# Performance work log

Hardware: AMD Instinct MI355X
Metric: run time of the kernel (lower is better)

## Reference

```python
import jax, jax.numpy as jnp
import numpy as np
from jax import lax

D, H_HEADS, DEPTH, E, HID, P, NCLS = 768, 12, 12, 4, 3072, 16, 1000

def _ln(x, w, b, eps=1e-5):
    m = x.mean(-1, keepdims=True)
    v = ((x - m) ** 2).mean(-1, keepdims=True)
    return (x - m) * lax.rsqrt(v + eps) * w + b

def setup_inputs() -> dict:
    key = jax.random.key(0)
    ks = jax.random.split(key, 16)
    s = 0.02
    inp = {
        'x': jax.random.normal(ks[0], (32, 3, 224, 224), jnp.float32),
        'conv_w': jax.random.normal(ks[1], (D, 3, P, P), jnp.float32) * s,
        'conv_b': jnp.zeros((D,), jnp.float32),
        'cls_token': jnp.zeros((1, 1, D), jnp.float32),
        'pos_embed': jax.random.normal(ks[2], (1, 197, D), jnp.float32) * s,
        'ln1_w': jnp.ones((DEPTH, D), jnp.float32),
        'ln1_b': jnp.zeros((DEPTH, D), jnp.float32),
        'qkv_w': jax.random.normal(ks[3], (DEPTH, 3 * D, D), jnp.float32) * s,
        'qkv_b': jnp.zeros((DEPTH, 3 * D), jnp.float32),
        'out_w': jax.random.normal(ks[4], (DEPTH, D, D), jnp.float32) * s,
        'out_b': jnp.zeros((DEPTH, D), jnp.float32),
        'ln2_w': jnp.ones((DEPTH, D), jnp.float32),
        'ln2_b': jnp.zeros((DEPTH, D), jnp.float32),
        'gate_w': jax.random.normal(ks[5], (DEPTH, E, D), jnp.float32) * s,
        'gate_b': jnp.zeros((DEPTH, E), jnp.float32),
        'e1_w': jax.random.normal(ks[6], (DEPTH, E, HID, D), jnp.float32) * s,
        'e1_b': jnp.zeros((DEPTH, E, HID), jnp.float32),
        'e2_w': jax.random.normal(ks[7], (DEPTH, E, D, HID), jnp.float32) * s,
        'e2_b': jnp.zeros((DEPTH, E, D), jnp.float32),
        'fnorm_w': jnp.ones((D,), jnp.float32),
        'fnorm_b': jnp.zeros((D,), jnp.float32),
        'head_w': jax.random.normal(ks[8], (NCLS, D), jnp.float32) * s,
        'head_b': jnp.zeros((NCLS,), jnp.float32),
    }
    return inp

def reference(x, conv_w, conv_b, cls_token, pos_embed, ln1_w, ln1_b, qkv_w, qkv_b,
              out_w, out_b, ln2_w, ln2_b, gate_w, gate_b, e1_w, e1_b, e2_w, e2_b,
              fnorm_w, fnorm_b, head_w, head_b):
    B = x.shape[0]
    # patch embedding: conv stride=patch, then flatten -> [B, N, D]
    x = lax.conv_general_dilated(x, conv_w, (P, P), 'VALID',
                                 dimension_numbers=('NCHW', 'OIHW', 'NCHW'))
    x = x + conv_b[None, :, None, None]
    x = x.reshape(B, D, -1).transpose(0, 2, 1)
    x = jnp.concatenate([jnp.broadcast_to(cls_token, (B, 1, D)), x], axis=1)
    x = x + pos_embed
    N = x.shape[1]
    hd = D // H_HEADS
    for i in range(DEPTH):
        # --- attention ---
        h = x
        y = _ln(x, ln1_w[i], ln1_b[i])
        qkv = y @ qkv_w[i].T + qkv_b[i]                      # [B,N,3D]
        q, k, v = jnp.split(qkv, 3, axis=-1)
        q = q.reshape(B, N, H_HEADS, hd).transpose(0, 2, 1, 3) / jnp.sqrt(hd).astype(x.dtype)
        k = k.reshape(B, N, H_HEADS, hd).transpose(0, 2, 1, 3)
        v = v.reshape(B, N, H_HEADS, hd).transpose(0, 2, 1, 3)
        attn = jax.nn.softmax(jnp.einsum('bhqd,bhkd->bhqk', q, k), axis=-1)
        ctx = jnp.einsum('bhqk,bhkd->bhqd', attn, v).transpose(0, 2, 1, 3).reshape(B, N, D)
        x = h + (ctx @ out_w[i].T + out_b[i])
        # --- MoE MLP (dense: all experts computed then masked, top_k=1) ---
        h = x
        y = _ln(x, ln2_w[i], ln2_b[i])
        gate = y @ gate_w[i].T + gate_b[i]                   # [B,N,E]
        topk_scores, topk_idx = lax.top_k(gate, 1)           # [B,N,1]
        score = jax.nn.softmax(topk_scores, axis=-1)[..., 0]  # [B,N] (==1 for k=1)
        h1 = jax.nn.gelu(jnp.einsum('bnd,ehd->benh', y, e1_w[i])
                         + e1_b[i][None, :, None, :], approximate=False)  # [B,E,N,HID]
        oe = jnp.einsum('benh,edh->bend', h1, e2_w[i]) + e2_b[i][None, :, None, :]
        mask = jax.nn.one_hot(topk_idx[..., 0], E, dtype=y.dtype)  # [B,N,E]
        moe = jnp.einsum('bne,bend->bnd', mask * score[..., None], oe)
        x = h + moe
    x = _ln(x, fnorm_w, fnorm_b)
    cls = x[:, 0]
    return cls @ head_w.T + head_b
```

## Files before the change

kernel.cpp:

```cpp
#include <hip/hip_runtime.h>
#include <hip/hip_bf16.h>
#include <math.h>

#define D_MODEL 768
#define SEQ     197
#define BATCH   32
#define NTOK    (BATCH*SEQ)
#define NHEAD   12
#define HDIM    64
#define NEXP    4
#define HID_N   3072
#define DEPTH_N 12

typedef __attribute__((ext_vector_type(4))) float f32x4;
typedef __attribute__((ext_vector_type(8))) short bf16x8;
typedef __attribute__((ext_vector_type(2))) unsigned int u32x2;

static __device__ __forceinline__ unsigned short f2bf(float f){
  unsigned int u = __builtin_bit_cast(unsigned int, f);
  u += 0x7FFFu + ((u >> 16) & 1u);
  return (unsigned short)(u >> 16);
}
static __device__ __forceinline__ void split_bf(float x, unsigned short& h, unsigned short& l){
  h = f2bf(x);
  float hf = __builtin_bit_cast(float, (unsigned)h << 16);
  l = f2bf(x - hf);
}

static __device__ __forceinline__ float wred_sum(float v){
  #pragma unroll
  for (int off = 32; off; off >>= 1) v += __shfl_down(v, off);
  return v;
}

static __device__ __forceinline__ int xcd_map(int orig, int nwg){
  int q = nwg >> 3, r = nwg & 7;
  int xcd = orig & 7, idx = orig >> 3;
  return (xcd < r ? xcd*(q+1) : r*(q+1) + (xcd-r)*q) + idx;
}

template<int MODE>
__global__ __launch_bounds__(256, 2) void gemm_bf16x3(
    const float* __restrict__ A, const float* __restrict__ W,
    const float* __restrict__ bias, const float* __restrict__ resid,
    float* __restrict__ C, const float* __restrict__ pos,
    const int* __restrict__ toks, const int* __restrict__ cnts,
    const int* __restrict__ offs, const int* __restrict__ tiles,
    int M, int N, int K)
{
  const int tid = threadIdx.x;
  const int NB = N >> 7;
  const int nm = gridDim.x / NB;
  const int lg = xcd_map(blockIdx.x, gridDim.x);
  const int mt = lg % nm, nb = lg / nm;

  int cnt = M, base = 0, m0;
  if (MODE == 2 || MODE == 3){
    if (mt >= tiles[0]) return;
    const int e = tiles[1 + 2*mt];
    m0 = tiles[2 + 2*mt];
    cnt  = cnts[e];
    base = offs[e];
    W    += (size_t)e * N * K;
    bias += (size_t)e * N;
  } else {
    m0 = mt * 128;
  }
  const int n0 = nb * 128;

  __shared__ __align__(16) unsigned short Ah[128][40];
  __shared__ __align__(16) unsigned short Al[128][40];
  __shared__ __align__(16) unsigned short Wh[128][40];
  __shared__ __align__(16) unsigned short Wl[128][40];

  const int srow = tid >> 3;
  const int kc   = (tid & 7) * 4;
  const float* pA[4];
  const float* pW[4];
  size_t pbase4[4];
  #pragma unroll
  for (int p = 0; p < 4; p++){
    int r  = p * 32 + srow;
    int gm = m0 + r;
    if (MODE == 0 || MODE == 1) pA[p] = (gm < M)   ? A + (size_t)gm * K : nullptr;
    if (MODE == 2)              pA[p] = (gm < cnt) ? A + (size_t)toks[base + gm] * K : nullptr;
    if (MODE == 3)              pA[p] = (gm < cnt) ? A + (size_t)(base + gm) * K : nullptr;
    if (MODE == 4){
      int b_ = gm / 196, pp = gm - b_ * 196;
      int py = pp / 14,  px = pp - py * 14;
      pbase4[p] = (size_t)b_ * 150528 + (size_t)py * 3584 + (size_t)px * 16;
      pA[p] = A;
    }
    pW[p] = W + (size_t)(n0 + r) * K;
  }

  const int NT = K >> 5;
  const int lane = tid & 63, wid = tid >> 6;
  const int wr = wid >> 1, wc = wid & 1;
  const int lr = lane & 15, lq = lane >> 4;

  f32x4 acc[4][4] = {};

  auto LOAD = [&](int kt, f32x4* vA, f32x4* vW){
    const int k = kt * 32 + kc;
    #pragma unroll
    for (int p = 0; p < 4; p++){
      if (MODE == 4){
        size_t off = pbase4[p] + (size_t)(k >> 8) * 50176
                   + (size_t)((k >> 4) & 15) * 224 + (size_t)(k & 15);
        vA[p] = *reinterpret_cast<const f32x4*>(A + off);
      } else {
        vA[p] = pA[p] ? *reinterpret_cast<const f32x4*>(pA[p] + k)
                      : f32x4{0.f, 0.f, 0.f, 0.f};
      }
      vW[p] = *reinterpret_cast<const f32x4*>(pW[p] + k);
    }
  };
  auto STORE = [&](const f32x4* vA, const f32x4* vW){
    #pragma unroll
    for (int p = 0; p < 4; p++){
      int r = p * 32 + srow;
      unsigned short h0,h1,h2,h3,l0,l1,l2,l3;
      split_bf(vA[p][0], h0, l0); split_bf(vA[p][1], h1, l1);
      split_bf(vA[p][2], h2, l2); split_bf(vA[p][3], h3, l3);
      u32x2 hp, lp;
      hp[0] = (unsigned)h0 | ((unsigned)h1 << 16); hp[1] = (unsigned)h2 | ((unsigned)h3 << 16);
      lp[0] = (unsigned)l0 | ((unsigned)l1 << 16); lp[1] = (unsigned)l2 | ((unsigned)l3 << 16);
      *reinterpret_cast<u32x2*>(&Ah[r][kc]) = hp;
      *reinterpret_cast<u32x2*>(&Al[r][kc]) = lp;
      split_bf(vW[p][0], h0, l0); split_bf(vW[p][1], h1, l1);
      split_bf(vW[p][2], h2, l2); split_bf(vW[p][3], h3, l3);
      hp[0] = (unsigned)h0 | ((unsigned)h1 << 16); hp[1] = (unsigned)h2 | ((unsigned)h3 << 16);
      lp[0] = (unsigned)l0 | ((unsigned)l1 << 16); lp[1] = (unsigned)l2 | ((unsigned)l3 << 16);
      *reinterpret_cast<u32x2*>(&Wh[r][kc]) = hp;
      *reinterpret_cast<u32x2*>(&Wl[r][kc]) = lp;
    }
  };

  {
    f32x4 cA[4], cW[4];
    LOAD(0, cA, cW);
    STORE(cA, cW);
  }
  __syncthreads();

  for (int t = 0; t < NT; t++){
    f32x4 nA[4], nW[4];
    if (t + 1 < NT) LOAD(t + 1, nA, nW);
    bf16x8 afh[4], afl[4], bfh[4], bfl[4];
    #pragma unroll
    for (int mi = 0; mi < 4; mi++){
      afh[mi] = *reinterpret_cast<const bf16x8*>(&Ah[wr*64 + mi*16 + lr][lq*8]);
      afl[mi] = *reinterpret_cast<const bf16x8*>(&Al[wr*64 + mi*16 + lr][lq*8]);
    }
    #pragma unroll
    for (int nj = 0; nj < 4; nj++){
      bfh[nj] = *reinterpret_cast<const bf16x8*>(&Wh[wc*64 + nj*16 + lr][lq*8]);
      bfl[nj] = *reinterpret_cast<const bf16x8*>(&Wl[wc*64 + nj*16 + lr][lq*8]);
    }
    #pragma unroll
    for (int mi = 0; mi < 4; mi++)
      #pragma unroll
      for (int nj = 0; nj < 4; nj++){
        acc[mi][nj] = __builtin_amdgcn_mfma_f32_16x16x32_bf16(afh[mi], bfh[nj], acc[mi][nj], 0, 0, 0);
        acc[mi][nj] = __builtin_amdgcn_mfma_f32_16x16x32_bf16(afh[mi], bfl[nj], acc[mi][nj], 0, 0, 0);
        acc[mi][nj] = __builtin_amdgcn_mfma_f32_16x16x32_bf16(afl[mi], bfh[nj], acc[mi][nj], 0, 0, 0);
      }
    __syncthreads();
    if (t + 1 < NT){
      STORE(nA, nW);
      __syncthreads();
    }
  }

  #pragma unroll
  for (int nj = 0; nj < 4; nj++){
    const int ncol = n0 + wc*64 + nj*16 + lr;
    const float bv = bias[ncol];
    #pragma unroll
    for (int mi = 0; mi < 4; mi++){
      const int mb = m0 + wr*64 + mi*16 + lq*4;
      #pragma unroll
      for (int j = 0; j < 4; j++){
        const int m = mb + j;
        float v = acc[mi][nj][j] + bv;
        if (MODE == 0){
          if (m < M) C[(size_t)m * N + ncol] = v;
        }
        if (MODE == 1){
          if (m < M) C[(size_t)m * N + ncol] = v + resid[(size_t)m * N + ncol];
        }
        if (MODE == 2){
          if (m < cnt){
            v = 0.5f * v * (1.f + erff(v * 0.70710678118f));
            C[(size_t)(base + m) * N + ncol] = v;
          }
        }
        if (MODE == 3){
          if (m < cnt){
            int tok = toks[base + m];
            C[(size_t)tok * N + ncol] += v;
          }
        }
        if (MODE == 4){
          int b_ = m / 196, pp = m - b_ * 196;
          C[((size_t)b_ * 197 + 1 + pp) * D_MODEL + ncol] =
              v + pos[(size_t)(1 + pp) * D_MODEL + ncol];
        }
      }
    }
  }
}

__global__ __launch_bounds__(256) void cls_init(const float* __restrict__ cls_tk,
                                                const float* __restrict__ pos,
                                                float* __restrict__ xt){
  const int b = blockIdx.x, tid = threadIdx.x;
  for (int d = tid; d < D_MODEL; d += 256)
    xt[((size_t)b*SEQ)*D_MODEL + d] = cls_tk[d] + pos[d];
}

__global__ __launch_bounds__(256) void ln_kernel(const float* __restrict__ x, size_t xstride,
                                                 const float* __restrict__ w,
                                                 const float* __restrict__ b,
                                                 float* __restrict__ y, size_t ystride){
  const int t = blockIdx.x;
  const int tid = threadIdx.x;
  const float* row = x + (size_t)t*xstride;
  float v0 = row[tid], v1 = row[tid+256], v2 = row[tid+512];
  __shared__ float red[4];
  float s = wred_sum(v0+v1+v2);
  if ((tid & 63) == 0) red[tid>>6] = s;
  __syncthreads();
  const float mean = (red[0]+red[1]+red[2]+red[3]) * (1.f/768.f);
  const float d0 = v0-mean, d1 = v1-mean, d2 = v2-mean;
  __syncthreads();
  float q = wred_sum(d0*d0 + d1*d1 + d2*d2);
  if ((tid & 63) == 0) red[tid>>6] = q;
  __syncthreads();
  const float var = (red[0]+red[1]+red[2]+red[3]) * (1.f/768.f);
  const float inv = rsqrtf(var + 1e-5f);
  float* yr = y + (size_t)t*ystride;
  yr[tid]     = d0*inv*w[tid]     + b[tid];
  yr[tid+256] = d1*inv*w[tid+256] + b[tid+256];
  yr[tid+512] = d2*inv*w[tid+512] + b[tid+512];
}

__global__ __launch_bounds__(256, 3) void attn_f32(const float* __restrict__ qkv,
                                                   float* __restrict__ ctx){
  const int qt = blockIdx.x, h = blockIdx.y, b = blockIdx.z;
  const int tid = threadIdx.x;
  const int tx = tid & 15, ty = tid >> 4;
  __shared__ float Qs[64][65];
  __shared__ float KPs[64][65];
  __shared__ float Vs[64][65];
  const size_t rs = 3*D_MODEL;
  const float* base = qkv + (size_t)b*SEQ*rs + (size_t)h*HDIM;

  #pragma unroll
  for (int it = 0; it < 16; it++){
    int idx = tid + it*256;
    int r = idx >> 6, c = idx & 63;
    int gq = qt*64 + r;
    float v = (gq < SEQ) ? base[(size_t)gq*rs + c] : 0.f;
    Qs[r][c] = v * 0.125f;
  }
  float m_run[4], l_run[4], o[4][4];
  #pragma unroll
  for (int i = 0; i < 4; i++){
    m_run[i] = -3.0e38f; l_run[i] = 0.f;
    #pragma unroll
    for (int j = 0; j < 4; j++) o[i][j] = 0.f;
  }
  __syncthreads();

  for (int kt = 0; kt < 4; kt++){
    #pragma unroll
    for (int it = 0; it < 16; it++){
      int idx = tid + it*256;
      int r = idx >> 6, c = idx & 63;
      int gk = kt*64 + r;
      float kv = (gk < SEQ) ? base[(size_t)gk*rs + D_MODEL   + c] : 0.f;
      float vv = (gk < SEQ) ? base[(size_t)gk*rs + 2*D_MODEL + c] : 0.f;
      KPs[r][c] = kv;
      Vs[r][c]  = vv;
    }
    __syncthreads();
    float s[4][4] = {};
    for (int d = 0; d < 64; d++){
      float qv[4], kv2[4];
      #pragma unroll
      for (int i = 0; i < 4; i++) qv[i]  = Qs[ty*4+i][d];
      #pragma unroll
      for (int j = 0; j < 4; j++) kv2[j] = KPs[tx*4+j][d];
      #pragma unroll
      for (int i = 0; i < 4; i++)
        #pragma unroll
        for (int j = 0; j < 4; j++) s[i][j] += qv[i]*kv2[j];
    }
    #pragma unroll
    for (int j = 0; j < 4; j++){
      if (kt*64 + tx*4 + j >= SEQ){
        #pragma unroll
        for (int i = 0; i < 4; i++) s[i][j] = -3.0e38f;
      }
    }
    float scale[4];
    #pragma unroll
    for (int i = 0; i < 4; i++){
      float mt = fmaxf(fmaxf(s[i][0], s[i][1]), fmaxf(s[i][2], s[i][3]));
      #pragma unroll
      for (int msk = 1; msk <= 8; msk <<= 1) mt = fmaxf(mt, __shfl_xor(mt, msk));
      float mnew = fmaxf(m_run[i], mt);
      scale[i] = __expf(m_run[i] - mnew);
      float ls = 0.f;
      #pragma unroll
      for (int j = 0; j < 4; j++){ s[i][j] = __expf(s[i][j] - mnew); ls += s[i][j]; }
      #pragma unroll
      for (int msk = 1; msk <= 8; msk <<= 1) ls += __shfl_xor(ls, msk);
      l_run[i] = l_run[i]*scale[i] + ls;
      m_run[i] = mnew;
    }
    __syncthreads();
    #pragma unroll
    for (int i = 0; i < 4; i++)
      #pragma unroll
      for (int j = 0; j < 4; j++) KPs[ty*4+i][tx*4+j] = s[i][j];
    __syncthreads();
    #pragma unroll
    for (int i = 0; i < 4; i++)
      #pragma unroll
      for (int j = 0; j < 4; j++) o[i][j] *= scale[i];
    for (int k = 0; k < 64; k++){
      float pv[4], vv[4];
      #pragma unroll
      for (int i = 0; i < 4; i++) pv[i] = KPs[ty*4+i][k];
      #pragma unroll
      for (int j = 0; j < 4; j++) vv[j] = Vs[k][tx*4+j];
      #pragma unroll
      for (int i = 0; i < 4; i++)
        #pragma unroll
        for (int j = 0; j < 4; j++) o[i][j] += pv[i]*vv[j];
    }
    __syncthreads();
  }
  #pragma unroll
  for (int i = 0; i < 4; i++){
    int q = qt*64 + ty*4 + i;
    if (q < SEQ){
      float inv = 1.f / l_run[i];
      #pragma unroll
      for (int j = 0; j < 4; j++)
        ctx[((size_t)(b*SEQ + q))*D_MODEL + h*HDIM + tx*4 + j] = o[i][j]*inv;
    }
  }
}

__global__ __launch_bounds__(256) void gate_kernel(const float* __restrict__ y,
                                                   const float* __restrict__ gw,
                                                   const float* __restrict__ gb,
                                                   int* __restrict__ eidx){
  const int t = blockIdx.x;
  const int tid = threadIdx.x;
  const int e = tid >> 6, lane = tid & 63;
  const float* row = y + (size_t)t*D_MODEL;
  const float* wrow = gw + (size_t)e*D_MODEL;
  float acc = 0.f;
  for (int k = lane; k < D_MODEL; k += 64) acc += row[k]*wrow[k];
  acc = wred_sum(acc);
  __shared__ float sc[NEXP];
  if (lane == 0) sc[e] = acc + gb[e];
  __syncthreads();
  if (tid == 0){
    int best = 0; float bv = sc[0];
    #pragma unroll
    for (int k = 1; k < NEXP; k++) if (sc[k] > bv){ bv = sc[k]; best = k; }
    eidx[t] = best;
  }
}

__global__ void zero_counts(int* c){ if (threadIdx.x < 3*NEXP) c[threadIdx.x] = 0; }

__global__ __launch_bounds__(256) void count_kernel(const int* __restrict__ eidx, int* counts){
  int i = blockIdx.x*256 + threadIdx.x;
  if (i < NTOK) atomicAdd(&counts[eidx[i]], 1);
}

__global__ void offsets_kernel(const int* counts, int* offs, int* cursor, int* tiles){
  if (threadIdx.x == 0){
    int o = 0, n = 0;
    for (int e = 0; e < NEXP; e++){
      offs[e] = o; cursor[e] = o;
      for (int m0 = 0; m0 < counts[e]; m0 += 128){
        tiles[1+2*n] = e; tiles[2+2*n] = m0; n++;
      }
      o += counts[e];
    }
    tiles[0] = n;
  }
}

__global__ __launch_bounds__(256) void scatter_kernel(const int* __restrict__ eidx,
                                                      int* cursor, int* __restrict__ toks){
  int i = blockIdx.x*256 + threadIdx.x;
  if (i < NTOK){ int pos = atomicAdd(&cursor[eidx[i]], 1); toks[pos] = i; }
}

__global__ __launch_bounds__(256) void gemm_f32(const float* __restrict__ A,
                                                const float* __restrict__ W,
                                                const float* __restrict__ bias,
                                                const float* __restrict__ resid,
                                                float* __restrict__ C,
                                                int M, int N, int K){
  const int m0 = blockIdx.x*64, bn = blockIdx.y*64;
  const int tid = threadIdx.x;
  const int tx = tid & 15, ty = tid >> 4;
  __shared__ float As[16][65];
  __shared__ float Ws[16][65];
  float acc[4][4] = {};
  for (int k0 = 0; k0 < K; k0 += 16){
    #pragma unroll
    for (int i = 0; i < 4; i++){
      int idx = tid + i*256;
      int k = idx & 15, m = idx >> 4;
      As[k][m] = (m0+m < M) ? A[(size_t)(m0+m)*K + k0 + k] : 0.f;
      Ws[k][m] = (bn+m < N) ? W[(size_t)(bn+m)*K + k0 + k] : 0.f;
    }
    __syncthreads();
    #pragma unroll
    for (int kk = 0; kk < 16; kk++){
      float a0 = As[kk][ty*4+0], a1 = As[kk][ty*4+1], a2 = As[kk][ty*4+2], a3 = As[kk][ty*4+3];
      float w0 = Ws[kk][tx*4+0], w1 = Ws[kk][tx*4+1], w2 = Ws[kk][tx*4+2], w3 = Ws[kk][tx*4+3];
      acc[0][0] += a0*w0; acc[0][1] += a0*w1; acc[0][2] += a0*w2; acc[0][3] += a0*w3;
      acc[1][0] += a1*w0; acc[1][1] += a1*w1; acc[1][2] += a1*w2; acc[1][3] += a1*w3;
      acc[2][0] += a2*w0; acc[2][1] += a2*w1; acc[2][2] += a2*w2; acc[2][3] += a2*w3;
      acc[3][0] += a3*w0; acc[3][1] += a3*w1; acc[3][2] += a3*w2; acc[3][3] += a3*w3;
    }
    __syncthreads();
  }
  #pragma unroll
  for (int i = 0; i < 4; i++){
    int m = m0 + ty*4 + i;
    if (m >= M) continue;
    #pragma unroll
    for (int j = 0; j < 4; j++){
      int n = bn + tx*4 + j;
      if (n >= N) continue;
      float v = acc[i][j];
      if (bias)  v += bias[n];
      if (resid) v += resid[(size_t)m*N + n];
      C[(size_t)m*N + n] = v;
    }
  }
}

extern "C" void kernel_launch(void* const* d_in, const int* in_sizes, int n_in,
                              void* d_out, int out_size, void* d_ws, size_t ws_size,
                              hipStream_t stream){
  const float* x      = (const float*)d_in[0];
  const float* conv_w = (const float*)d_in[1];
  const float* conv_b = (const float*)d_in[2];
  const float* cls_tk = (const float*)d_in[3];
  const float* pos    = (const float*)d_in[4];
  const float* ln1w   = (const float*)d_in[5];
  const float* ln1b   = (const float*)d_in[6];
  const float* qkvw   = (const float*)d_in[7];
  const float* qkvb   = (const float*)d_in[8];
  const float* outw   = (const float*)d_in[9];
  const float* outb   = (const float*)d_in[10];
  const float* ln2w   = (const float*)d_in[11];
  const float* ln2b   = (const float*)d_in[12];
  const float* gatew  = (const float*)d_in[13];
  const float* gateb  = (const float*)d_in[14];
  const float* e1w    = (const float*)d_in[15];
  const float* e1b    = (const float*)d_in[16];
  const float* e2w    = (const float*)d_in[17];
  const float* e2b    = (const float*)d_in[18];
  const float* fnw    = (const float*)d_in[19];
  const float* fnb    = (const float*)d_in[20];
  const float* headw  = (const float*)d_in[21];
  const float* headb  = (const float*)d_in[22];
  float* out = (float*)d_out;

  float* ws    = (float*)d_ws;
  float* xt    = ws;
  float* y     = xt  + (size_t)NTOK*D_MODEL;
  float* qkv   = y   + (size_t)NTOK*D_MODEL;
  float* ctx   = qkv + (size_t)NTOK*3*D_MODEL;
  float* h1    = ctx + (size_t)NTOK*D_MODEL;
  float* clsln = h1  + (size_t)NTOK*HID_N;
  int*   eidx   = (int*)(clsln + (size_t)BATCH*D_MODEL);
  int*   toks   = eidx + NTOK;
  int*   counts = toks + NTOK;
  int*   offs   = counts + NEXP;
  int*   cursor = offs + NEXP;
  int*   tiles  = cursor + NEXP;

  dim3 b256(256);

  gemm_bf16x3<4><<<dim3(49*6), b256, 0, stream>>>(x, conv_w, conv_b, nullptr, xt,
      pos, nullptr, nullptr, nullptr, nullptr, 6272, D_MODEL, 768);
  cls_init<<<dim3(BATCH), b256, 0, stream>>>(cls_tk, pos, xt);

  for (int i = 0; i < DEPTH_N; i++){
    ln_kernel<<<dim3(NTOK), b256, 0, stream>>>(xt, D_MODEL,
        ln1w + (size_t)i*D_MODEL, ln1b + (size_t)i*D_MODEL, y, D_MODEL);
    gemm_bf16x3<0><<<dim3(50*18), b256, 0, stream>>>(y,
        qkvw + (size_t)i*3*D_MODEL*D_MODEL, qkvb + (size_t)i*3*D_MODEL,
        nullptr, qkv, nullptr, nullptr, nullptr, nullptr, nullptr, NTOK, 3*D_MODEL, D_MODEL);
    attn_f32<<<dim3(4, NHEAD, BATCH), b256, 0, stream>>>(qkv, ctx);
    gemm_bf16x3<1><<<dim3(50*6), b256, 0, stream>>>(ctx,
        outw + (size_t)i*D_MODEL*D_MODEL, outb + (size_t)i*D_MODEL,
        xt, xt, nullptr, nullptr, nullptr, nullptr, nullptr, NTOK, D_MODEL, D_MODEL);
    ln_kernel<<<dim3(NTOK), b256, 0, stream>>>(xt, D_MODEL,
        ln2w + (size_t)i*D_MODEL, ln2b + (size_t)i*D_MODEL, y, D_MODEL);
    gate_kernel<<<dim3(NTOK), b256, 0, stream>>>(y,
        gatew + (size_t)i*NEXP*D_MODEL, gateb + (size_t)i*NEXP, eidx);
    zero_counts<<<1, 64, 0, stream>>>(counts);
    count_kernel<<<dim3((NTOK+255)/256), b256, 0, stream>>>(eidx, counts);
    offsets_kernel<<<1, 64, 0, stream>>>(counts, offs, cursor, tiles);
    scatter_kernel<<<dim3((NTOK+255)/256), b256, 0, stream>>>(eidx, cursor, toks);
    gemm_bf16x3<2><<<dim3(53*(HID_N/128)), b256, 0, stream>>>(y,
        e1w + (size_t)i*NEXP*HID_N*D_MODEL, e1b + (size_t)i*NEXP*HID_N,
        nullptr, h1, nullptr, toks, counts, offs, tiles, NTOK, HID_N, D_MODEL);
    gemm_bf16x3<3><<<dim3(53*(D_MODEL/128)), b256, 0, stream>>>(h1,
        e2w + (size_t)i*NEXP*D_MODEL*HID_N, e2b + (size_t)i*NEXP*D_MODEL,
        nullptr, xt, nullptr, toks, counts, offs, tiles, NTOK, D_MODEL, HID_N);
  }

  ln_kernel<<<dim3(BATCH), b256, 0, stream>>>(xt, (size_t)SEQ*D_MODEL, fnw, fnb, clsln, D_MODEL);
  gemm_f32<<<dim3(1, 16), b256, 0, stream>>>(clsln, headw, headb, nullptr, out, BATCH, 1000, D_MODEL);
}
```

Baseline: 11.02 ms.

## Pre-split operands to bf16 hi/lo and stream GEMM tiles via async LDS loads

Weights and the input image are converted once per call into separate bf16 high and low arrays. The LayerNorm, attention and first expert GEMM now write their outputs directly in split form. The GEMM kernel no longer loads fp32 and converts it inside the main loop: it stages pre-split tiles with global_load_lds into double-buffered, XOR-swizzled shared memory, with waitcnt/barrier pipelining. This removes per-tile conversion ALU work and register staging, and lets global loads overlap the MFMAs. In exchange, each call pays a large conversion pass over all weights plus extra workspace traffic.

After: 11.10 ms. No clear change (+0.8%).

```diff
diff --git a/kernel.cpp b/kernel.cpp
--- a/kernel.cpp
+++ b/kernel.cpp
@@ -14,14 +14,15 @@
 
 typedef __attribute__((ext_vector_type(4))) float f32x4;
 typedef __attribute__((ext_vector_type(8))) short bf16x8;
-typedef __attribute__((ext_vector_type(2))) unsigned int u32x2;
-
-static __device__ __forceinline__ unsigned short f2bf(float f){
+typedef __attribute__((ext_vector_type(4))) unsigned short u16x4;
+typedef unsigned short u16;
+
+static __device__ __forceinline__ u16 f2bf(float f){
   unsigned int u = __builtin_bit_cast(unsigned int, f);
   u += 0x7FFFu + ((u >> 16) & 1u);
-  return (unsigned short)(u >> 16);
-}
-static __device__ __forceinline__ void split_bf(float x, unsigned short& h, unsigned short& l){
+  return (u16)(u >> 16);
+}
+static __device__ __forceinline__ void split_bf(float x, u16& h, u16& l){
   h = f2bf(x);
   float hf = __builtin_bit_cast(float, (unsigned)h << 16);
   l = f2bf(x - hf);
@@ -39,11 +40,32 @@
   return (xcd < r ? xcd*(q+1) : r*(q+1) + (xcd-r)*q) + idx;
 }
 
+static __device__ __forceinline__ void gld16(const u16* g, u16* l){
+  __builtin_amdgcn_global_load_lds(
+      (const __attribute__((address_space(1))) unsigned int*)g,
+      (__attribute__((address_space(3))) unsigned int*)l, 16, 0, 0);
+}
+
+__global__ __launch_bounds__(256) void split_many(const float* __restrict__ src,
+                                                  u16* __restrict__ hi,
+                                                  u16* __restrict__ lo, long n4){
+  for (long i = blockIdx.x*256L + threadIdx.x; i < n4; i += (long)gridDim.x*256){
+    f32x4 v = *reinterpret_cast<const f32x4*>(src + i*4);
+    u16x4 h, l;
+    #pragma unroll
+    for (int j = 0; j < 4; j++){ u16 hh, ll; split_bf(v[j], hh, ll); h[j]=hh; l[j]=ll; }
+    *reinterpret_cast<u16x4*>(hi + i*4) = h;
+    *reinterpret_cast<u16x4*>(lo + i*4) = l;
+  }
+}
+
 template<int MODE>
-__global__ __launch_bounds__(256, 2) void gemm_bf16x3(
-    const float* __restrict__ A, const float* __restrict__ W,
+__global__ __launch_bounds__(256, 2) void gemm_split(
+    const u16* __restrict__ Ahp, const u16* __restrict__ Alp,
+    const u16* __restrict__ Whp, const u16* __restrict__ Wlp,
     const float* __restrict__ bias, const float* __restrict__ resid,
     float* __restrict__ C, const float* __restrict__ pos,
+    u16* __restrict__ Chi, u16* __restrict__ Clo,
     const int* __restrict__ toks, const int* __restrict__ cnts,
     const int* __restrict__ offs, const int* __restrict__ tiles,
     int M, int N, int K)
@@ -61,102 +83,103 @@
     m0 = tiles[2 + 2*mt];
     cnt  = cnts[e];
     base = offs[e];
-    W    += (size_t)e * N * K;
+    Whp  += (size_t)e * N * K;
+    Wlp  += (size_t)e * N * K;
     bias += (size_t)e * N;
   } else {
     m0 = mt * 128;
   }
   const int n0 = nb * 128;
 
-  __shared__ __align__(16) unsigned short Ah[128][40];
-  __shared__ __align__(16) unsigned short Al[128][40];
-  __shared__ __align__(16) unsigned short Wh[128][40];
-  __shared__ __align__(16) unsigned short Wl[128][40];
-
-  const int srow = tid >> 3;
-  const int kc   = (tid & 7) * 4;
-  const float* pA[4];
-  const float* pW[4];
-  size_t pbase4[4];
-  #pragma unroll
-  for (int p = 0; p < 4; p++){
-    int r  = p * 32 + srow;
-    int gm = m0 + r;
-    if (MODE == 0 || MODE == 1) pA[p] = (gm < M)   ? A + (size_t)gm * K : nullptr;
-    if (MODE == 2)              pA[p] = (gm < cnt) ? A + (size_t)toks[base + gm] * K : nullptr;
-    if (MODE == 3)              pA[p] = (gm < cnt) ? A + (size_t)(base + gm) * K : nullptr;
+  __shared__ __align__(16) u16 lds[2][4][4096];
+
+  const int lane = tid & 63, wid = tid >> 6;
+  const int i0 = wid*128 + lane;
+  const int r0 = i0 >> 2, r1 = r0 + 16;
+  const int x0 = (i0 & 3) ^ ((r0 >> 1) & 3);
+  const int x1 = (i0 & 3) ^ ((r1 >> 1) & 3);
+  const int d0 = wid*1024, d1 = wid*1024 + 512;
+
+  size_t aA0 = 0, aA1 = 0, pb0 = 0, pb1 = 0;
+  {
+    const int gm0 = m0 + r0, gm1 = m0 + r1;
+    if (MODE == 0 || MODE == 1){
+      aA0 = (size_t)(gm0 < M ? gm0 : 0) * K + x0*8;
+      aA1 = (size_t)(gm1 < M ? gm1 : 0) * K + x1*8;
+    }
+    if (MODE == 2){
+      aA0 = (size_t)(gm0 < cnt ? toks[base+gm0] : 0) * K + x0*8;
+      aA1 = (size_t)(gm1 < cnt ? toks[base+gm1] : 0) * K + x1*8;
+    }
+    if (MODE == 3){
+      aA0 = (size_t)(gm0 < cnt ? base+gm0 : 0) * K + x0*8;
+      aA1 = (size_t)(gm1 < cnt ? base+gm1 : 0) * K + x1*8;
+    }
     if (MODE == 4){
-      int b_ = gm / 196, pp = gm - b_ * 196;
-      int py = pp / 14,  px = pp - py * 14;
-      pbase4[p] = (size_t)b_ * 150528 + (size_t)py * 3584 + (size_t)px * 16;
-      pA[p] = A;
-    }
-    pW[p] = W + (size_t)(n0 + r) * K;
-  }
-
-  const int NT = K >> 5;
-  const int lane = tid & 63, wid = tid >> 6;
+      int b_ = gm0 / 196, pp = gm0 - b_*196;
+      pb0 = (size_t)b_*150528 + (size_t)(pp/14)*3584 + (size_t)(pp%14)*16;
+      b_ = gm1 / 196; pp = gm1 - b_*196;
+      pb1 = (size_t)b_*150528 + (size_t)(pp/14)*3584 + (size_t)(pp%14)*16;
+    }
+  }
+  const size_t aW0 = (size_t)(n0 + r0) * K + x0*8;
+  const size_t aW1 = (size_t)(n0 + r1) * K + x1*8;
+
+  auto STAGE = [&](int buf, int t){
+    const int k0 = t * 32;
+    if (MODE == 4){
+      const int kq0 = k0 + x0*8, kq1 = k0 + x1*8;
+      size_t a0 = pb0 + (size_t)(kq0>>8)*50176 + (size_t)((kq0>>4)&15)*224 + (size_t)(kq0&15);
+      size_t a1 = pb1 + (size_t)(kq1>>8)*50176 + (size_t)((kq1>>4)&15)*224 + (size_t)(kq1&15);
+      gld16(Ahp + a0, &lds[buf][0][d0]); gld16(Ahp + a1, &lds[buf][0][d1]);
+      gld16(Alp + a0, &lds[buf][1][d0]); gld16(Alp + a1, &lds[buf][1][d1]);
+    } else {
+      gld16(Ahp + aA0 + k0, &lds[buf][0][d0]); gld16(Ahp + aA1 + k0, &lds[buf][0][d1]);
+      gld16(Alp + aA0 + k0, &lds[buf][1][d0]); gld16(Alp + aA1 + k0, &lds[buf][1][d1]);
+    }
+    gld16(Whp + aW0 + k0, &lds[buf][2][d0]); gld16(Whp + aW1 + k0, &lds[buf][2][d1]);
+    gld16(Wlp + aW0 + k0, &lds[buf][3][d0]); gld16(Wlp + aW1 + k0, &lds[buf][3][d1]);
+  };
+
   const int wr = wid >> 1, wc = wid & 1;
   const int lr = lane & 15, lq = lane >> 4;
-
+  int cA[4], cW[4];
+  #pragma unroll
+  for (int mi = 0; mi < 4; mi++){
+    int ra = wr*64 + mi*16 + lr;
+    cA[mi] = (4*ra + (lq ^ ((ra>>1)&3))) * 8;
+  }
+  #pragma unroll
+  for (int nj = 0; nj < 4; nj++){
+    int rw = wc*64 + nj*16 + lr;
+    cW[nj] = (4*rw + (lq ^ ((rw>>1)&3))) * 8;
+  }
+
+  const int NT = K >> 5;
   f32x4 acc[4][4] = {};
 
-  auto LOAD = [&](int kt, f32x4* vA, f32x4* vW){
-    const int k = kt * 32 + kc;
-    #pragma unroll
-    for (int p = 0; p < 4; p++){
-      if (MODE == 4){
-        size_t off = pbase4[p] + (size_t)(k >> 8) * 50176
-                   + (size_t)((k >> 4) & 15) * 224 + (size_t)(k & 15);
-        vA[p] = *reinterpret_cast<const f32x4*>(A + off);
-      } else {
-        vA[p] = pA[p] ? *reinterpret_cast<const f32x4*>(pA[p] + k)
-                      : f32x4{0.f, 0.f, 0.f, 0.f};
-      }
-      vW[p] = *reinterpret_cast<const f32x4*>(pW[p] + k);
-    }
-  };
-  auto STORE = [&](const f32x4* vA, const f32x4* vW){
-    #pragma unroll
-    for (int p = 0; p < 4; p++){
-      int r = p * 32 + srow;
-      unsigned short h0,h1,h2,h3,l0,l1,l2,l3;
-      split_bf(vA[p][0], h0, l0); split_bf(vA[p][1], h1, l1);
-      split_bf(vA[p][2], h2, l2); split_bf(vA[p][3], h3, l3);
-      u32x2 hp, lp;
-      hp[0] = (unsigned)h0 | ((unsigned)h1 << 16); hp[1] = (unsigned)h2 | ((unsigned)h3 << 16);
-      lp[0] = (unsigned)l0 | ((unsigned)l1 << 16); lp[1] = (unsigned)l2 | ((unsigned)l3 << 16);
-      *reinterpret_cast<u32x2*>(&Ah[r][kc]) = hp;
-      *reinterpret_cast<u32x2*>(&Al[r][kc]) = lp;
-      split_bf(vW[p][0], h0, l0); split_bf(vW[p][1], h1, l1);
-      split_bf(vW[p][2], h2, l2); split_bf(vW[p][3], h3, l3);
-      hp[0] = (unsigned)h0 | ((unsigned)h1 << 16); hp[1] = (unsigned)h2 | ((unsigned)h3 << 16);
-      lp[0] = (unsigned)l0 | ((unsigned)l1 << 16); lp[1] = (unsigned)l2 | ((unsigned)l3 << 16);
-      *reinterpret_cast<u32x2*>(&Wh[r][kc]) = hp;
-      *reinterpret_cast<u32x2*>(&Wl[r][kc]) = lp;
-    }
-  };
-
-  {
-    f32x4 cA[4], cW[4];
-    LOAD(0, cA, cW);
-    STORE(cA, cW);
-  }
-  __syncthreads();
-
+  STAGE(0, 0);
   for (int t = 0; t < NT; t++){
-    f32x4 nA[4], nW[4];
-    if (t + 1 < NT) LOAD(t + 1, nA, nW);
+    const int buf = t & 1;
+    if (t + 1 < NT){
+      STAGE(buf ^ 1, t + 1);
+      asm volatile("s_waitcnt vmcnt(8)" ::: "memory");
+    } else {
+      asm volatile("s_waitcnt vmcnt(0)" ::: "memory");
+    }
+    __builtin_amdgcn_s_barrier();
+    asm volatile("" ::: "memory");
+    const u16* L = &lds[buf][0][0];
     bf16x8 afh[4], afl[4], bfh[4], bfl[4];
     #pragma unroll
     for (int mi = 0; mi < 4; mi++){
-      afh[mi] = *reinterpret_cast<const bf16x8*>(&Ah[wr*64 + mi*16 + lr][lq*8]);
-      afl[mi] = *reinterpret_cast<const bf16x8*>(&Al[wr*64 + mi*16 + lr][lq*8]);
+      afh[mi] = *reinterpret_cast<const bf16x8*>(L + cA[mi]);
+      afl[mi] = *reinterpret_cast<const bf16x8*>(L + 4096 + cA[mi]);
     }
     #pragma unroll
     for (int nj = 0; nj < 4; nj++){
-      bfh[nj] = *reinterpret_cast<const bf16x8*>(&Wh[wc*64 + nj*16 + lr][lq*8]);
-      bfl[nj] = *reinterpret_cast<const bf16x8*>(&Wl[wc*64 + nj*16 + lr][lq*8]);
+      bfh[nj] = *reinterpret_cast<const bf16x8*>(L + 2*4096 + cW[nj]);
+      bfl[nj] = *reinterpret_cast<const bf16x8*>(L + 3*4096 + cW[nj]);
     }
     #pragma unroll
     for (int mi = 0; mi < 4; mi++)
@@ -166,11 +189,8 @@
         acc[mi][nj] = __builtin_amdgcn_mfma_f32_16x16x32_bf16(afh[mi], bfl[nj], acc[mi][nj], 0, 0, 0);
         acc[mi][nj] = __builtin_amdgcn_mfma_f32_16x16x32_bf16(afl[mi], bfh[nj], acc[mi][nj], 0, 0, 0);
       }
-    __syncthreads();
-    if (t + 1 < NT){
-      STORE(nA, nW);
-      __syncthreads();
-    }
+    asm volatile("" ::: "memory");
+    __builtin_amdgcn_s_barrier();
   }
 
   #pragma unroll
@@ -193,7 +213,9 @@
         if (MODE == 2){
           if (m < cnt){
             v = 0.5f * v * (1.f + erff(v * 0.70710678118f));
-            C[(size_t)(base + m) * N + ncol] = v;
+            u16 h, l; split_bf(v, h, l);
+            Chi[(size_t)(base + m) * N + ncol] = h;
+            Clo[(size_t)(base + m) * N + ncol] = l;
           }
         }
         if (MODE == 3){
@@ -223,7 +245,8 @@
 __global__ __launch_bounds__(256) void ln_kernel(const float* __restrict__ x, size_t xstride,
                                                  const float* __restrict__ w,
                                                  const float* __restrict__ b,
-                                                 float* __restrict__ y, size_t ystride){
+                                                 float* __restrict__ y, size_t ystride,
+                                                 u16* __restrict__ yh, u16* __restrict__ yl){
   const int t = blockIdx.x;
   const int tid = threadIdx.x;
   const float* row = x + (size_t)t*xstride;
@@ -240,14 +263,23 @@
   __syncthreads();
   const float var = (red[0]+red[1]+red[2]+red[3]) * (1.f/768.f);
   const float inv = rsqrtf(var + 1e-5f);
+  float o0 = d0*inv*w[tid]     + b[tid];
+  float o1 = d1*inv*w[tid+256] + b[tid+256];
+  float o2 = d2*inv*w[tid+512] + b[tid+512];
   float* yr = y + (size_t)t*ystride;
-  yr[tid]     = d0*inv*w[tid]     + b[tid];
-  yr[tid+256] = d1*inv*w[tid+256] + b[tid+256];
-  yr[tid+512] = d2*inv*w[tid+512] + b[tid+512];
+  yr[tid] = o0; yr[tid+256] = o1; yr[tid+512] = o2;
+  if (yh){
+    u16 h, l;
+    size_t rb = (size_t)t*768;
+    split_bf(o0, h, l); yh[rb+tid]     = h; yl[rb+tid]     = l;
+    split_bf(o1, h, l); yh[rb+tid+256] = h; yl[rb+tid+256] = l;
+    split_bf(o2, h, l); yh[rb+tid+512] = h; yl[rb+tid+512] = l;
+  }
 }
 
 __global__ __launch_bounds__(256, 3) void attn_f32(const float* __restrict__ qkv,
-                                                   float* __restrict__ ctx){
+                                                   u16* __restrict__ ctxh,
+                                                   u16* __restrict__ ctxl){
   const int qt = blockIdx.x, h = blockIdx.y, b = blockIdx.z;
   const int tid = threadIdx.x;
   const int tx = tid & 15, ty = tid >> 4;
@@ -350,8 +382,12 @@
     if (q < SEQ){
       float inv = 1.f / l_run[i];
       #pragma unroll
-      for (int j = 0; j < 4; j++)
-        ctx[((size_t)(b*SEQ + q))*D_MODEL + h*HDIM + tx*4 + j] = o[i][j]*inv;
+      for (int j = 0; j < 4; j++){
+        u16 hh, ll;
+        split_bf(o[i][j]*inv, hh, ll);
+        size_t idx = ((size_t)(b*SEQ + q))*D_MODEL + h*HDIM + tx*4 + j;
+        ctxh[idx] = hh; ctxl[idx] = ll;
+      }
     }
   }
 }
@@ -486,48 +522,77 @@
   float* xt    = ws;
   float* y     = xt  + (size_t)NTOK*D_MODEL;
   float* qkv   = y   + (size_t)NTOK*D_MODEL;
-  float* ctx   = qkv + (size_t)NTOK*3*D_MODEL;
-  float* h1    = ctx + (size_t)NTOK*D_MODEL;
-  float* clsln = h1  + (size_t)NTOK*HID_N;
+  float* clsln = qkv + (size_t)NTOK*3*D_MODEL;
   int*   eidx   = (int*)(clsln + (size_t)BATCH*D_MODEL);
   int*   toks   = eidx + NTOK;
   int*   counts = toks + NTOK;
   int*   offs   = counts + NEXP;
   int*   cursor = offs + NEXP;
   int*   tiles  = cursor + NEXP;
+  u16* up = (u16*)(((size_t)(tiles + 120) + 15) & ~(size_t)15);
+  const size_t nY  = (size_t)NTOK*D_MODEL;
+  const size_t nH1 = (size_t)NTOK*HID_N;
+  const size_t nX  = (size_t)BATCH*3*224*224;
+  const size_t nCW = 768*768;
+  const size_t nQW = (size_t)DEPTH_N*3*D_MODEL*D_MODEL;
+  const size_t nOW = (size_t)DEPTH_N*D_MODEL*D_MODEL;
+  const size_t nE1 = (size_t)DEPTH_N*NEXP*HID_N*D_MODEL;
+  const size_t nE2 = (size_t)DEPTH_N*NEXP*D_MODEL*HID_N;
+  u16 *yh = up,      *yl = yh + nY;
+  u16 *ch = yl + nY, *cl = ch + nY;
+  u16 *h1h = cl + nY, *h1l = h1h + nH1;
+  u16 *xh = h1l + nH1, *xl = xh + nX;
+  u16 *cwh = xl + nX,  *cwl = cwh + nCW;
+  u16 *qwh = cwl + nCW, *qwl = qwh + nQW;
+  u16 *owh = qwl + nQW, *owl = owh + nOW;
+  u16 *e1h = owl + nOW, *e1l = e1h + nE1;
+  u16 *e2h = e1l + nE1, *e2l = e2h + nE2;
 
   dim3 b256(256);
 
-  gemm_bf16x3<4><<<dim3(49*6), b256, 0, stream>>>(x, conv_w, conv_b, nullptr, xt,
-      pos, nullptr, nullptr, nullptr, nullptr, 6272, D_MODEL, 768);
+  split_many<<<2048, b256, 0, stream>>>(x,      xh,  xl,  (long)(nX/4));
+  split_many<<<2048, b256, 0, stream>>>(conv_w, cwh, cwl, (long)(nCW/4));
+  split_many<<<2048, b256, 0, stream>>>(qkvw,   qwh, qwl, (long)(nQW/4));
+  split_many<<<2048, b256, 0, stream>>>(outw,   owh, owl, (long)(nOW/4));
+  split_many<<<2048, b256, 0, stream>>>(e1w,    e1h, e1l, (long)(nE1/4));
+  split_many<<<2048, b256, 0, stream>>>(e2w,    e2h, e2l, (long)(nE2/4));
+
+  gemm_split<4><<<dim3(49*6), b256, 0, stream>>>(xh, xl, cwh, cwl,
+      conv_b, nullptr, xt, pos, nullptr, nullptr,
+      nullptr, nullptr, nullptr, nullptr, 6272, D_MODEL, 768);
   cls_init<<<dim3(BATCH), b256, 0, stream>>>(cls_tk, pos, xt);
 
   for (int i = 0; i < DEPTH_N; i++){
     ln_kernel<<<dim3(NTOK), b256, 0, stream>>>(xt, D_MODEL,
-        ln1w + (size_t)i*D_MODEL, ln1b + (size_t)i*D_MODEL, y, D_MODEL);
-    gemm_bf16x3<0><<<dim3(50*18), b256, 0, stream>>>(y,
-        qkvw + (size_t)i*3*D_MODEL*D_MODEL, qkvb + (size_t)i*3*D_MODEL,
-        nullptr, qkv, nullptr, nullptr, nullptr, nullptr, nullptr, NTOK, 3*D_MODEL, D_MODEL);
-    attn_f32<<<dim3(4, NHEAD, BATCH), b256, 0, stream>>>(qkv, ctx);
-    gemm_bf16x3<1><<<dim3(50*6), b256, 0, stream>>>(ctx,
-        outw + (size_t)i*D_MODEL*D_MODEL, outb + (size_t)i*D_MODEL,
-        xt, xt, nullptr, nullptr, nullptr, nullptr, nullptr, NTOK, D_MODEL, D_MODEL);
+        ln1w + (size_t)i*D_MODEL, ln1b + (size_t)i*D_MODEL, y, D_MODEL, yh, yl);
+    gemm_split<0><<<dim3(50*18), b256, 0, stream>>>(yh, yl,
+        qwh + (size_t)i*3*D_MODEL*D_MODEL, qwl + (size_t)i*3*D_MODEL*D_MODEL,
+        qkvb + (size_t)i*3*D_MODEL, nullptr, qkv, nullptr, nullptr, nullptr,
+        nullptr, nullptr, nullptr, nullptr, NTOK, 3*D_MODEL, D_MODEL);
+    attn_f32<<<dim3(4, NHEAD, BATCH), b256, 0, stream>>>(qkv, ch, cl);
+    gemm_split<1><<<dim3(50*6), b256, 0, stream>>>(ch, cl,
+        owh + (size_t)i*D_MODEL*D_MODEL, owl + (size_t)i*D_MODEL*D_MODEL,
+        outb + (size_t)i*D_MODEL, xt, xt, nullptr, nullptr, nullptr,
+        nullptr, nullptr, nullptr, nullptr, NTOK, D_MODEL, D_MODEL);
     ln_kernel<<<dim3(NTOK), b256, 0, stream>>>(xt, D_MODEL,
-        ln2w + (size_t)i*D_MODEL, ln2b + (size_t)i*D_MODEL, y, D_MODEL);
+        ln2w + (size_t)i*D_MODEL, ln2b + (size_t)i*D_MODEL, y, D_MODEL, yh, yl);
     gate_kernel<<<dim3(NTOK), b256, 0, stream>>>(y,
         gatew + (size_t)i*NEXP*D_MODEL, gateb + (size_t)i*NEXP, eidx);
     zero_counts<<<1, 64, 0, stream>>>(counts);
     count_kernel<<<dim3((NTOK+255)/256), b256, 0, stream>>>(eidx, counts);
     offsets_kernel<<<1, 64, 0, stream>>>(counts, offs, cursor, tiles);
     scatter_kernel<<<dim3((NTOK+255)/256), b256, 0, stream>>>(eidx, cursor, toks);
-    gemm_bf16x3<2><<<dim3(53*(HID_N/128)), b256, 0, stream>>>(y,
-        e1w + (size_t)i*NEXP*HID_N*D_MODEL, e1b + (size_t)i*NEXP*HID_N,
-        nullptr, h1, nullptr, toks, counts, offs, tiles, NTOK, HID_N, D_MODEL);
-    gemm_bf16x3<3><<<dim3(53*(D_MODEL/128)), b256, 0, stream>>>(h1,
-        e2w + (size_t)i*NEXP*D_MODEL*HID_N, e2b + (size_t)i*NEXP*D_MODEL,
-        nullptr, xt, nullptr, toks, counts, offs, tiles, NTOK, D_MODEL, HID_N);
-  }
-
-  ln_kernel<<<dim3(BATCH), b256, 0, stream>>>(xt, (size_t)SEQ*D_MODEL, fnw, fnb, clsln, D_MODEL);
+    gemm_split<2><<<dim3(53*(HID_N/128)), b256, 0, stream>>>(yh, yl,
+        e1h + (size_t)i*NEXP*HID_N*D_MODEL, e1l + (size_t)i*NEXP*HID_N*D_MODEL,
+        e1b + (size_t)i*NEXP*HID_N, nullptr, nullptr, nullptr, h1h, h1l,
+        toks, counts, offs, tiles, NTOK, HID_N, D_MODEL);
+    gemm_split<3><<<dim3(53*(D_MODEL/128)), b256, 0, stream>>>(h1h, h1l,
+        e2h + (size_t)i*NEXP*D_MODEL*HID_N, e2l + (size_t)i*NEXP*D_MODEL*HID_N,
+        e2b + (size_t)i*NEXP*D_MODEL, nullptr, xt, nullptr, nullptr, nullptr,
+        toks, counts, offs, tiles, NTOK, D_MODEL, HID_N);
+  }
+
+  ln_kernel<<<dim3(BATCH), b256, 0, stream>>>(xt, (size_t)SEQ*D_MODEL, fnw, fnb,
+      clsln, D_MODEL, nullptr, nullptr);
   gemm_f32<<<dim3(1, 16), b256, 0, stream>>>(clsln, headw, headb, nullptr, out, BATCH, 1000, D_MODEL);
 }
```
